# Performance work log

Hardware: AMD Instinct MI355X
Metric: run time of the kernel (lower is better)

Reference implementation:

```python
import jax, jax.numpy as jnp
import numpy as np

NUM_ITERATIONS = 3  # init kwarg num_iterations
EPS = 1e-12         # F.normalize eps


def _k_means_routing(priors, num_iterations):
    # priors: (B, O, I, J) = (batch, out_capsules, in_capsules, out_length)
    out = priors.mean(axis=-2, keepdims=True)  # (B, O, 1, J)
    for _ in range(num_iterations):
        norm = jnp.sqrt(jnp.sum(out * out, axis=-1, keepdims=True))
        out_n = out / jnp.maximum(norm, EPS)                       # L2 normalize over J
        logits = jnp.sum(priors * out_n, axis=-1, keepdims=True)   # (B, O, I, 1) dot similarity
        coef = jax.nn.softmax(logits, axis=-2)                     # softmax over in_capsules
        out = jnp.sum(coef * priors, axis=-2, keepdims=True)       # (B, O, 1, J)
    return jnp.squeeze(out, axis=-2)  # (B, O, J); squash=False so no squash


def setup_inputs() -> dict:
    key = jax.random.key(0)
    k1, k2 = jax.random.split(key)
    B, I, L = 32, 512, 64   # batch, in_capsules, in_length
    O, J = 128, 64          # out_capsules, out_length
    x = jax.random.normal(k1, (B, I, L), dtype=jnp.float32)
    # xavier_uniform for weight (O, J, L): fan_in = J*L... torch uses size(1)*prod(rest)
    bound = float(np.sqrt(6.0 / (J * L + O * L)))
    weight = jax.random.uniform(k2, (O, J, L), dtype=jnp.float32, minval=-bound, maxval=bound)
    return {"x": x, "weight": weight}


def reference(x, weight):
    # priors[b,o,i,j] = sum_l weight[o,j,l] * x[b,i,l]  -> (B, O, I, J)
    priors = jnp.einsum('ojl,bil->boij', weight, x)
    return _k_means_routing(priors, NUM_ITERATIONS)
```

## Files before the change

kernel.cpp:

```cpp
#include <hip/hip_runtime.h>
#include <hip/hip_fp16.h>


#define CB 32
#define CI 512
#define CL 64
#define CO 128
#define OPB 16
#define NT 1024

typedef _Float16 half8 __attribute__((ext_vector_type(8)));
typedef float f32x4 __attribute__((ext_vector_type(4)));

static __device__ __forceinline__ _Float16 half_sel(uint v, int sh) {
  union { unsigned short s; _Float16 h; } c;
  c.s = (unsigned short)(v >> sh);
  return c.h;
}

__global__ __launch_bounds__(256) void caps_gram(const float* __restrict__ wg,
                                                 __half2* __restrict__ Gq) {
  const int o = blockIdx.x;
  const int t = threadIdx.x;
  __shared__ float wl[64 * 65];
  __shared__ float gl[64 * 65];
#pragma unroll
  for (int k = 0; k < 16; ++k) {
    int f = t + 256 * k;
    int j = f >> 6, l = f & 63;
    wl[j * 65 + l] = wg[(o << 12) + f];
  }
  __syncthreads();
  const int l1 = t >> 2;
  const int l2b = (t & 3) << 4;
  float acc[16];
#pragma unroll
  for (int m = 0; m < 16; ++m) acc[m] = 0.f;
#pragma unroll 4
  for (int j = 0; j < 64; ++j) {
    float wa = wl[j * 65 + l1];
#pragma unroll
    for (int m = 0; m < 16; ++m) acc[m] += wa * wl[j * 65 + l2b + m];
  }
#pragma unroll
  for (int m = 0; m < 16; ++m) gl[l1 * 65 + l2b + m] = acc[m];
  __syncthreads();
#pragma unroll
  for (int j = 0; j < 8; ++j) {
    int e = t + 256 * j;
    int k = e >> 8;
    int l = (e >> 2) & 63;
    int qq = e & 3;
    int l2 = 8 * k + 2 * qq;
    Gq[(o << 11) + e] = __floats2half2_rn(gl[l2 * 65 + l], gl[(l2 + 1) * 65 + l]);
  }
}

__global__ __launch_bounds__(NT, 4) void caps_main(const float* __restrict__ xg,
                                                   const float* __restrict__ wg,
                                                   const __half2* __restrict__ Gq,
                                                   float* __restrict__ outg) {
  const int b = blockIdx.y;
  const int obase = blockIdx.x * OPB;
  const int t = threadIdx.x;
  const int w = t >> 6;
  const int lane = t & 63;
  const int g = lane >> 4;
  const int o15 = lane & 15;

  __shared__ __align__(16) _Float16 xs[CI * CL];
  __shared__ __align__(16) _Float16 xT[CL * CI];
  __shared__ __align__(16) _Float16 coefT[OPB * CI];
  __shared__ __align__(16) _Float16 wn16[OPB * CL];
  __shared__ __align__(16) float xc_s[OPB * CL];
  __shared__ float se_part[OPB * OPB];
  float* const xcpart = reinterpret_cast<float*>(coefT);
  char* const xs_b = reinterpret_cast<char*>(xs);
  char* const xT_b = reinterpret_cast<char*>(xT);
  char* const cf_b = reinterpret_cast<char*>(coefT);
  char* const wn_b = reinterpret_cast<char*>(wn16);

  const int qh = w >> 2, nt = w & 3;
  const int lcol = nt * 16 + o15;

  {
    const float4* xg4 = reinterpret_cast<const float4*>(xg + b * (CI * CL));
#pragma unroll
    for (int k = 0; k < 4; ++k) {
      int f = t + NT * k;
      int i = f >> 3, lu = f & 7;
      float4 a = xg4[2 * f];
      float4 c = xg4[2 * f + 1];
      union { _Float16 h[8]; uint4 u; } cv;
      cv.h[0] = (_Float16)a.x; cv.h[1] = (_Float16)a.y;
      cv.h[2] = (_Float16)a.z; cv.h[3] = (_Float16)a.w;
      cv.h[4] = (_Float16)c.x; cv.h[5] = (_Float16)c.y;
      cv.h[6] = (_Float16)c.z; cv.h[7] = (_Float16)c.w;
      int off = ((i >> 4) * 4 + (lu >> 1)) * 512 + (i & 15) * 32 + (lu & 1) * 16;
      *reinterpret_cast<uint4*>(xs_b + off) = cv.u;
    }
  }
  __syncthreads();

  uint4 gq0, gq1, gq2, gq3, gq4, gq5, gq6, gq7;
  const uint4* Gp = reinterpret_cast<const uint4*>(Gq) +
                    (((obase + w) << 3) << 6) + lane;
#define PREFETCH_GQ()                                                       \
  {                                                                         \
    gq0 = Gp[0 * 64]; gq1 = Gp[1 * 64]; gq2 = Gp[2 * 64]; gq3 = Gp[3 * 64]; \
    gq4 = Gp[4 * 64]; gq5 = Gp[5 * 64]; gq6 = Gp[6 * 64]; gq7 = Gp[7 * 64]; \
  }

  {
    const uint* xrd32 = reinterpret_cast<const uint*>(
                            xs_b + nt * 512 + ((o15 & 8) << 1)) +
                        ((o15 & 7) >> 1);
    const int sh = (o15 & 1) << 4;
    float xbs = 0.f;
#define GATHW(K)                                                            \
  {                                                                         \
    int P = qh * 16 + (K)*4 + g;                                            \
    const uint* xk = xrd32 + (P >> 1) * 512 + (P & 1) * 64;                 \
    uint d0 = xk[0], d1 = xk[8], d2 = xk[16], d3 = xk[24];                  \
    uint d4 = xk[32], d5 = xk[40], d6 = xk[48], d7 = xk[56];                \
    union { _Float16 h[8]; uint4 u; } fv;                                   \
    fv.h[0] = half_sel(d0, sh); fv.h[1] = half_sel(d1, sh);                 \
    fv.h[2] = half_sel(d2, sh); fv.h[3] = half_sel(d3, sh);                 \
    fv.h[4] = half_sel(d4, sh); fv.h[5] = half_sel(d5, sh);                 \
    fv.h[6] = half_sel(d6, sh); fv.h[7] = half_sel(d7, sh);                 \
    xbs += (float)fv.h[0] + (float)fv.h[1] + (float)fv.h[2] +               \
           (float)fv.h[3] + (float)fv.h[4] + (float)fv.h[5] +               \
           (float)fv.h[6] + (float)fv.h[7];                                 \
    *reinterpret_cast<uint4*>(xT_b + lcol * 1024 +                          \
                              ((P ^ (lcol & 7)) << 4)) = fv.u;              \
  }
    GATHW(0) GATHW(1) GATHW(2) GATHW(3)
#undef GATHW
    xbs += __shfl_xor(xbs, 16, 64);
    xbs += __shfl_xor(xbs, 32, 64);
    if (lane < 16) xcpart[qh * 1024 + nt * 16 + lane] = xbs;
    PREFETCH_GQ();
  }
  __syncthreads();

  for (int pass = 0; pass < 4; ++pass) {
    if (pass > 0) {
      half8 bw0 = *reinterpret_cast<const half8*>(
          wn_b + o15 * 128 + ((g ^ (o15 & 7)) << 4));
      half8 bw1 = *reinterpret_cast<const half8*>(
          wn_b + o15 * 128 + (((4 + g) ^ (o15 & 7)) << 4));
      float sacc = 0.f;
#pragma unroll
      for (int ti = 0; ti < 2; ++ti) {
        const int st = 2 * w + ti;
        const int itb = st * 2048;
        half8 a0 = *reinterpret_cast<const half8*>(
            xs_b + itb + ((g >> 1) * 512) + o15 * 32 + ((g & 1) << 4));
        half8 a1 = *reinterpret_cast<const half8*>(
            xs_b + itb + ((2 + (g >> 1)) * 512) + o15 * 32 + ((g & 1) << 4));
        f32x4 d = {0.f, 0.f, 0.f, 0.f};
        d = __builtin_amdgcn_mfma_f32_16x16x32_f16(a0, bw0, d, 0, 0, 0);
        d = __builtin_amdgcn_mfma_f32_16x16x32_f16(a1, bw1, d, 0, 0, 0);
        float e0 = __expf(d[0]), e1 = __expf(d[1]);
        float e2 = __expf(d[2]), e3 = __expf(d[3]);
        sacc += (e0 + e1) + (e2 + e3);
        int p = st * 2 + (g >> 1);
        union { _Float16 h[4]; uint2 u; } pk;
        pk.h[0] = (_Float16)e0; pk.h[1] = (_Float16)e1;
        pk.h[2] = (_Float16)e2; pk.h[3] = (_Float16)e3;
        *reinterpret_cast<uint2*>(cf_b + o15 * 1024 + ((p ^ o15) << 4) +
                                  ((g & 1) << 3)) = pk.u;
      }
      sacc += __shfl_xor(sacc, 16, 64);
      sacc += __shfl_xor(sacc, 32, 64);
      if (lane < 16) se_part[w * 16 + lane] = sacc;
      __syncthreads();

      f32x4 d = {0.f, 0.f, 0.f, 0.f};
#define MFMAK(K)                                                            \
  {                                                                         \
    int p = qh * 16 + (K)*4 + g;                                            \
    half8 a = *reinterpret_cast<const half8*>(cf_b + o15 * 1024 +           \
                                              ((p ^ o15) << 4));            \
    half8 bv = *reinterpret_cast<const half8*>(xT_b + lcol * 1024 +         \
                                               ((p ^ (lcol & 7)) << 4));    \
    d = __builtin_amdgcn_mfma_f32_16x16x32_f16(a, bv, d, 0, 0, 0);          \
  }
      MFMAK(0) MFMAK(1) MFMAK(2) MFMAK(3)
#undef MFMAK
      if (pass < 3) PREFETCH_GQ();
      __syncthreads();
#pragma unroll
      for (int r = 0; r < 4; ++r)
        xcpart[qh * 1024 + (g * 4 + r) * 64 + lcol] = d[r];
    }
    __syncthreads();

    {
      float xcv;
      if (pass == 0) {
        xcv = (xcpart[lane] + xcpart[1024 + lane] + xcpart[2048 + lane] +
               xcpart[3072 + lane]) * (1.0f / 512.0f);
      } else {
        float se = 0.f;
#pragma unroll
        for (int j = 0; j < 16; ++j) se += se_part[j * 16 + w];
        float sxc = xcpart[w * 64 + lane] + xcpart[1024 + w * 64 + lane] +
                    xcpart[2048 + w * 64 + lane] + xcpart[3072 + w * 64 + lane];
        xcv = sxc / se;
      }
      xc_s[(w << 6) + lane] = xcv;
      if (pass < 3) {
        const float4* xc4 = reinterpret_cast<const float4*>(&xc_s[w << 6]);
        float u0 = 0.f, u1 = 0.f, u2 = 0.f, u3 = 0.f;
#define GDOT(K)                                                             \
  {                                                                         \
    float4 xa = xc4[2 * (K)], xb = xc4[2 * (K) + 1];                        \
    float2 h0 = __half22float2(*reinterpret_cast<const __half2*>(&gq##K.x)); \
    float2 h1 = __half22float2(*reinterpret_cast<const __half2*>(&gq##K.y)); \
    float2 h2 = __half22float2(*reinterpret_cast<const __half2*>(&gq##K.z)); \
    float2 h3 = __half22float2(*reinterpret_cast<const __half2*>(&gq##K.w)); \
    u0 += h0.x * xa.x; u1 += h0.y * xa.y;                                   \
    u2 += h1.x * xa.z; u3 += h1.y * xa.w;                                   \
    u0 += h2.x * xb.x; u1 += h2.y * xb.y;                                   \
    u2 += h3.x * xb.z; u3 += h3.y * xb.w;                                   \
  }
        GDOT(0) GDOT(1) GDOT(2) GDOT(3) GDOT(4) GDOT(5) GDOT(6) GDOT(7)
#undef GDOT
        float uv = (u0 + u1) + (u2 + u3);
        float sq = uv * xcv;
#pragma unroll
        for (int m = 32; m; m >>= 1) sq += __shfl_xor(sq, m, 64);
        float wnv = uv / fmaxf(sqrtf(fmaxf(sq, 0.f)), 1e-12f);
        union { _Float16 hf; unsigned short us; } wc;
        wc.hf = (_Float16)wnv;
        *reinterpret_cast<unsigned short*>(
            wn_b + w * 128 + (((lane >> 3) ^ (w & 7)) << 4) +
            ((lane & 7) << 1)) = wc.us;
      }
    }
    __syncthreads();
  }

  {
    const float* Wp = wg + ((((obase + w) << 6) + lane) << 6);
    float a0 = 0.f, a1 = 0.f, a2 = 0.f, a3 = 0.f;
#pragma unroll
    for (int k = 0; k < 16; ++k) {
      float4 wv = *reinterpret_cast<const float4*>(&Wp[k << 2]);
      float4 xv = *reinterpret_cast<const float4*>(&xc_s[(w << 6) + (k << 2)]);
      a0 += wv.x * xv.x; a1 += wv.y * xv.y;
      a2 += wv.z * xv.z; a3 += wv.w * xv.w;
    }
    outg[((b << 7) + obase + w) * 64 + lane] = (a0 + a1) + (a2 + a3);
  }
#undef PREFETCH_GQ
}

extern "C" void kernel_launch(void* const* d_in, const int* in_sizes, int n_in,
                              void* d_out, int out_size, void* d_ws, size_t ws_size,
                              hipStream_t stream) {
  const float* x = (const float*)d_in[0];
  const float* wgt = (const float*)d_in[1];
  float* out = (float*)d_out;
  __half2* Gq = (__half2*)d_ws;

  caps_gram<<<dim3(CO), dim3(256), 0, stream>>>(wgt, Gq);
  caps_main<<<dim3(CO / OPB, CB), dim3(NT), 0, stream>>>(x, wgt, Gq, out);
}
```

Measured before the change: 37.75 us.

## Split gram kernel across two blocks per capsule and trim routing register and reduction work

The gram kernel now runs two blocks per output capsule. Each block computes half of the l1 rows and writes packed half2 results straight to global memory, which removes the second shared buffer and a sync. The main kernel keeps only four prefetched Gram vectors in registers and loads the other four just before the dot, cutting register pressure. It also skips the softmax normalization in early passes, since the later L2 normalize cancels the scale, and reduces the exp-sum only in the final pass using shuffles. The trade-off is some global load latency that is no longer hidden by prefetch.

```diff
diff --git a/kernel.cpp b/kernel.cpp
--- a/kernel.cpp
+++ b/kernel.cpp
@@ -21,9 +21,9 @@
 __global__ __launch_bounds__(256) void caps_gram(const float* __restrict__ wg,
                                                  __half2* __restrict__ Gq) {
   const int o = blockIdx.x;
+  const int h = blockIdx.y;
   const int t = threadIdx.x;
   __shared__ float wl[64 * 65];
-  __shared__ float gl[64 * 65];
 #pragma unroll
   for (int k = 0; k < 16; ++k) {
     int f = t + 256 * k;
@@ -31,29 +31,23 @@
     wl[j * 65 + l] = wg[(o << 12) + f];
   }
   __syncthreads();
-  const int l1 = t >> 2;
-  const int l2b = (t & 3) << 4;
-  float acc[16];
-#pragma unroll
-  for (int m = 0; m < 16; ++m) acc[m] = 0.f;
+  const int l1 = h * 32 + (t >> 3);
+  const int kq = t & 7;
+  const int l2b = kq << 3;
+  float acc[8];
+#pragma unroll
+  for (int m = 0; m < 8; ++m) acc[m] = 0.f;
 #pragma unroll 4
   for (int j = 0; j < 64; ++j) {
     float wa = wl[j * 65 + l1];
 #pragma unroll
-    for (int m = 0; m < 16; ++m) acc[m] += wa * wl[j * 65 + l2b + m];
-  }
-#pragma unroll
-  for (int m = 0; m < 16; ++m) gl[l1 * 65 + l2b + m] = acc[m];
-  __syncthreads();
-#pragma unroll
-  for (int j = 0; j < 8; ++j) {
-    int e = t + 256 * j;
-    int k = e >> 8;
-    int l = (e >> 2) & 63;
-    int qq = e & 3;
-    int l2 = 8 * k + 2 * qq;
-    Gq[(o << 11) + e] = __floats2half2_rn(gl[l2 * 65 + l], gl[(l2 + 1) * 65 + l]);
-  }
+    for (int m = 0; m < 8; ++m) acc[m] += wa * wl[j * 65 + l2b + m];
+  }
+  union { __half2 h2[4]; uint4 u; } pk;
+#pragma unroll
+  for (int q = 0; q < 4; ++q)
+    pk.h2[q] = __floats2half2_rn(acc[2 * q], acc[2 * q + 1]);
+  reinterpret_cast<uint4*>(Gq)[(o << 9) + (kq << 6) + l1] = pk.u;
 }
 
 __global__ __launch_bounds__(NT, 4) void caps_main(const float* __restrict__ xg,
@@ -82,6 +76,10 @@
 
   const int qh = w >> 2, nt = w & 3;
   const int lcol = nt * 16 + o15;
+
+  const uint4* Gp = reinterpret_cast<const uint4*>(Gq) +
+                    ((obase + w) << 9) + lane;
+  uint4 ga0, ga1, ga2, ga3;
 
   {
     const float4* xg4 = reinterpret_cast<const float4*>(xg + b * (CI * CL));
@@ -101,15 +99,6 @@
     }
   }
   __syncthreads();
-
-  uint4 gq0, gq1, gq2, gq3, gq4, gq5, gq6, gq7;
-  const uint4* Gp = reinterpret_cast<const uint4*>(Gq) +
-                    (((obase + w) << 3) << 6) + lane;
-#define PREFETCH_GQ()                                                       \
-  {                                                                         \
-    gq0 = Gp[0 * 64]; gq1 = Gp[1 * 64]; gq2 = Gp[2 * 64]; gq3 = Gp[3 * 64]; \
-    gq4 = Gp[4 * 64]; gq5 = Gp[5 * 64]; gq6 = Gp[6 * 64]; gq7 = Gp[7 * 64]; \
-  }
 
   {
     const uint* xrd32 = reinterpret_cast<const uint*>(
@@ -139,7 +128,7 @@
     xbs += __shfl_xor(xbs, 16, 64);
     xbs += __shfl_xor(xbs, 32, 64);
     if (lane < 16) xcpart[qh * 1024 + nt * 16 + lane] = xbs;
-    PREFETCH_GQ();
+    ga0 = Gp[0]; ga1 = Gp[64]; ga2 = Gp[128]; ga3 = Gp[192];
   }
   __syncthreads();
 
@@ -171,11 +160,16 @@
         *reinterpret_cast<uint2*>(cf_b + o15 * 1024 + ((p ^ o15) << 4) +
                                   ((g & 1) << 3)) = pk.u;
       }
-      sacc += __shfl_xor(sacc, 16, 64);
-      sacc += __shfl_xor(sacc, 32, 64);
-      if (lane < 16) se_part[w * 16 + lane] = sacc;
+      if (pass == 3) {
+        sacc += __shfl_xor(sacc, 16, 64);
+        sacc += __shfl_xor(sacc, 32, 64);
+        if (lane < 16) se_part[w * 16 + lane] = sacc;
+      }
       __syncthreads();
 
+      if (pass < 3) {
+        ga0 = Gp[0]; ga1 = Gp[64]; ga2 = Gp[128]; ga3 = Gp[192];
+      }
       f32x4 d = {0.f, 0.f, 0.f, 0.f};
 #define MFMAK(K)                                                            \
   {                                                                         \
@@ -188,7 +182,6 @@
   }
       MFMAK(0) MFMAK(1) MFMAK(2) MFMAK(3)
 #undef MFMAK
-      if (pass < 3) PREFETCH_GQ();
       __syncthreads();
 #pragma unroll
       for (int r = 0; r < 4; ++r)
@@ -197,35 +190,44 @@
     __syncthreads();
 
     {
+      float sxc;
+      if (pass == 0) {
+        sxc = xcpart[lane] + xcpart[1024 + lane] + xcpart[2048 + lane] +
+              xcpart[3072 + lane];
+      } else {
+        sxc = xcpart[w * 64 + lane] + xcpart[1024 + w * 64 + lane] +
+              xcpart[2048 + w * 64 + lane] + xcpart[3072 + w * 64 + lane];
+      }
       float xcv;
-      if (pass == 0) {
-        xcv = (xcpart[lane] + xcpart[1024 + lane] + xcpart[2048 + lane] +
-               xcpart[3072 + lane]) * (1.0f / 512.0f);
+      if (pass == 3) {
+        float sp = se_part[(lane & 15) * 16 + w];
+        sp += __shfl_xor(sp, 1, 64);
+        sp += __shfl_xor(sp, 2, 64);
+        sp += __shfl_xor(sp, 4, 64);
+        sp += __shfl_xor(sp, 8, 64);
+        xcv = sxc / sp;
       } else {
-        float se = 0.f;
-#pragma unroll
-        for (int j = 0; j < 16; ++j) se += se_part[j * 16 + w];
-        float sxc = xcpart[w * 64 + lane] + xcpart[1024 + w * 64 + lane] +
-                    xcpart[2048 + w * 64 + lane] + xcpart[3072 + w * 64 + lane];
-        xcv = sxc / se;
+        xcv = sxc;
       }
       xc_s[(w << 6) + lane] = xcv;
       if (pass < 3) {
+        uint4 gb0 = Gp[256], gb1 = Gp[320], gb2 = Gp[384], gb3 = Gp[448];
         const float4* xc4 = reinterpret_cast<const float4*>(&xc_s[w << 6]);
         float u0 = 0.f, u1 = 0.f, u2 = 0.f, u3 = 0.f;
-#define GDOT(K)                                                             \
+#define GDOT(V, K)                                                          \
   {                                                                         \
     float4 xa = xc4[2 * (K)], xb = xc4[2 * (K) + 1];                        \
-    float2 h0 = __half22float2(*reinterpret_cast<const __half2*>(&gq##K.x)); \
-    float2 h1 = __half22float2(*reinterpret_cast<const __half2*>(&gq##K.y)); \
-    float2 h2 = __half22float2(*reinterpret_cast<const __half2*>(&gq##K.z)); \
-    float2 h3 = __half22float2(*reinterpret_cast<const __half2*>(&gq##K.w)); \
+    float2 h0 = __half22float2(*reinterpret_cast<const __half2*>(&V.x));    \
+    float2 h1 = __half22float2(*reinterpret_cast<const __half2*>(&V.y));    \
+    float2 h2 = __half22float2(*reinterpret_cast<const __half2*>(&V.z));    \
+    float2 h3 = __half22float2(*reinterpret_cast<const __half2*>(&V.w));    \
     u0 += h0.x * xa.x; u1 += h0.y * xa.y;                                   \
     u2 += h1.x * xa.z; u3 += h1.y * xa.w;                                   \
     u0 += h2.x * xb.x; u1 += h2.y * xb.y;                                   \
     u2 += h3.x * xb.z; u3 += h3.y * xb.w;                                   \
   }
-        GDOT(0) GDOT(1) GDOT(2) GDOT(3) GDOT(4) GDOT(5) GDOT(6) GDOT(7)
+        GDOT(ga0, 0) GDOT(ga1, 1) GDOT(ga2, 2) GDOT(ga3, 3)
+        GDOT(gb0, 4) GDOT(gb1, 5) GDOT(gb2, 6) GDOT(gb3, 7)
 #undef GDOT
         float uv = (u0 + u1) + (u2 + u3);
         float sq = uv * xcv;
@@ -254,7 +256,6 @@
     }
     outg[((b << 7) + obase + w) * 64 + lane] = (a0 + a1) + (a2 + a3);
   }
-#undef PREFETCH_GQ
 }
 
 extern "C" void kernel_launch(void* const* d_in, const int* in_sizes, int n_in,
@@ -265,6 +266,6 @@
   float* out = (float*)d_out;
   __half2* Gq = (__half2*)d_ws;
 
-  caps_gram<<<dim3(CO), dim3(256), 0, stream>>>(wgt, Gq);
+  caps_gram<<<dim3(CO, 2), dim3(256), 0, stream>>>(wgt, Gq);
   caps_main<<<dim3(CO / OPB, CB), dim3(NT), 0, stream>>>(x, wgt, Gq, out);
 }
```

Result: faster. 35.18 us (-6.8%).
